# Optimization experiments

Hardware: AMD Instinct MI355X
Metric: run time of the kernel (lower is better)

## Reference

```python
import jax, jax.numpy as jnp
import numpy as np

D_WIN = 6
SIGMA = D_WIN / 2.0  # sigma = D/2
EPS = 1e-6


def _ln(x, g, b):
    m = jnp.mean(x, -1, keepdims=True)
    v = jnp.var(x, -1, keepdims=True)
    return (x - m) / jnp.sqrt(v + EPS) * g + b


def _cross_attn(q, kv, Wq, Wkv, Wproj, bproj, nh):
    # standard multi-head cross attention, no qkv bias (qkv_bias=False)
    B, S, C = q.shape
    N = kv.shape[1]
    hd = C // nh
    scale = hd ** -0.5
    qh = (q @ Wq).reshape(B, S, nh, hd).transpose(0, 2, 1, 3) * scale
    kvh = (kv @ Wkv).reshape(B, N, 2, nh, hd).transpose(2, 0, 3, 1, 4)
    k, v = kvh[0], kvh[1]
    attn = jax.nn.softmax(jnp.einsum('bhsd,bhnd->bhsn', qh, k), -1)
    x = jnp.einsum('bhsn,bhnd->bhsd', attn, v).transpose(0, 2, 1, 3).reshape(B, S, C)
    return x @ Wproj + bproj


def setup_inputs() -> dict:
    key = jax.random.key(0)
    ks = jax.random.split(key, 32)
    B, S, C, H, W = 32, 128, 384, 8, 512

    def lin(k, i, o):
        return jax.random.normal(k, (i, o), jnp.float32) * 0.02

    inp = {
        'q': jax.random.normal(ks[0], (B, S, C), jnp.float32),
        'kv': jax.random.normal(ks[1], (B, H * W, C), jnp.float32),
        # main attention linears (qkv_bias=False)
        'Wq': lin(ks[2], C, C),
        'Wkv': lin(ks[3], C, 2 * C),
        'Wproj': lin(ks[4], C, C), 'bproj': jnp.zeros((C,), jnp.float32),
        # position predictor
        'Wp_w': lin(ks[5], C, C), 'Wp_b': jnp.zeros((C,), jnp.float32),
        'vp_w': lin(ks[6], C, 1), 'vp_b': jnp.zeros((1,), jnp.float32),
        'Wqpos': lin(ks[7], C, C), 'bqpos': jnp.zeros((C,), jnp.float32),
        # simplified RCTC decoder projection
        'Wrctc': lin(ks[8], C, C), 'brctc': jnp.zeros((C,), jnp.float32),
        # pt_to_question cross attention (2 heads)
        'ca1_Wq': lin(ks[9], C, C), 'ca1_Wkv': lin(ks[10], C, 2 * C),
        'ca1_Wproj': lin(ks[11], C, C), 'ca1_bproj': jnp.zeros((C,), jnp.float32),
        # pt_to_image cross attention (2 heads)
        'ca2_Wq': lin(ks[12], C, C), 'ca2_Wkv': lin(ks[13], C, 2 * C),
        'ca2_Wproj': lin(ks[14], C, C), 'ca2_bproj': jnp.zeros((C,), jnp.float32),
        # layernorms
        'g_q1': jnp.ones((C,), jnp.float32), 'b_q1': jnp.zeros((C,), jnp.float32),
        'g_kv1': jnp.ones((C,), jnp.float32), 'b_kv1': jnp.zeros((C,), jnp.float32),
        'g_q2': jnp.ones((C,), jnp.float32), 'b_q2': jnp.zeros((C,), jnp.float32),
        'g_kv2': jnp.ones((C,), jnp.float32), 'b_kv2': jnp.zeros((C,), jnp.float32),
        'sz_h': H, 'sz_w': W,
    }
    return inp


def reference(q, kv, Wq, Wkv, Wproj, bproj, Wp_w, Wp_b, vp_w, vp_b, Wqpos, bqpos,
              Wrctc, brctc, ca1_Wq, ca1_Wkv, ca1_Wproj, ca1_bproj,
              ca2_Wq, ca2_Wkv, ca2_Wproj, ca2_bproj,
              g_q1, b_q1, g_kv1, b_kv1, g_q2, b_q2, g_kv2, b_kv2, sz_h, sz_w):
    B, N, C = kv.shape
    S = q.shape[1]
    H, W = sz_h, sz_w
    nh = 1
    hd = C // nh
    scale = hd ** -0.5

    # RCTC decoder (simplified): (B,N,C) -> (B,C,H,W) -> collapse H -> (B,W,C) -> linear
    kv_img = kv.transpose(0, 2, 1).reshape(B, C, H, W)
    dec = kv_img.mean(axis=2).transpose(0, 2, 1)  # (B, W, C)
    dec = dec @ Wrctc + brctc

    qh = (q @ Wq).reshape(B, S, nh, hd).transpose(0, 2, 1, 3) * scale  # (B,nh,S,hd)
    kvh = (dec @ Wkv).reshape(B, W, 2, nh, hd).transpose(2, 0, 3, 1, 4)
    k, v = kvh[0], kvh[1]  # (B,nh,W,hd)

    # position prediction branch
    p = q @ Wqpos + bqpos
    p = _cross_attn(_ln(p, g_q1, b_q1), _ln(q, g_kv1, b_kv1),
                    ca1_Wq, ca1_Wkv, ca1_Wproj, ca1_bproj, 2)
    p = _cross_attn(_ln(p, g_q2, b_q2), _ln(dec, g_kv2, b_kv2),
                    ca2_Wq, ca2_Wkv, ca2_Wproj, ca2_bproj, 2)
    p_t = jax.nn.sigmoid(jnp.tanh(p @ Wp_w + Wp_b) @ vp_w + vp_b) * W  # (B,S,1)

    # Gaussian window mask around predicted position
    idx = jnp.arange(W, dtype=jnp.float32)[None, None, None, :]     # (1,1,1,W)
    pexp = p_t[:, None, :, :]                                        # (B,1,S,1)
    gauss = jnp.exp(-(idx - pexp) ** 2 / (2.0 * SIGMA ** 2))         # (B,1,S,W)

    attn = jnp.einsum('bhsd,bhwd->bhsw', qh, k) * gauss
    attn = jax.nn.softmax(attn, -1)
    x = jnp.einsum('bhsw,bhwd->bhsd', attn, v).transpose(0, 2, 1, 3).reshape(B, S, C)
    return x @ Wproj + bproj
```

## Files before the change

### kernel.cpp

```cpp
#include <hip/hip_runtime.h>
#include <hip/hip_bf16.h>
#include <math.h>

#define B_ 32
#define S_ 128
#define C_ 384
#define H_ 8
#define W_ 512
#define NKV 4096

typedef __attribute__((ext_vector_type(8))) short short8;
typedef __attribute__((ext_vector_type(4))) float floatx4;

static __device__ __forceinline__ ushort f2bf(float v) {
    __hip_bfloat16 h = __float2bfloat16(v);
    return *(ushort*)&h;
}
static __device__ __forceinline__ float ldf(const float* p, size_t i) { return p[i]; }
static __device__ __forceinline__ float ldf(const ushort* p, size_t i) {
    union { uint u; float f; } c; c.u = (uint)p[i] << 16; return c.f;
}

__global__ __launch_bounds__(256) void mean_kernel(const float* __restrict__ kv,
                                                   ushort* __restrict__ dec0b) {
    int v = blockIdx.x * blockDim.x + threadIdx.x;
    int total = B_ * W_ * (C_ / 4);
    if (v >= total) return;
    int c4  = v % (C_ / 4);
    int row = v / (C_ / 4);
    int b = row / W_;
    int w = row % W_;
    const float4* src = (const float4*)kv + (size_t)(b * NKV + w) * (C_ / 4) + c4;
    float4 s = {0.f, 0.f, 0.f, 0.f};
#pragma unroll
    for (int h = 0; h < H_; ++h) {
        float4 t = src[(size_t)h * W_ * (C_ / 4)];
        s.x += t.x; s.y += t.y; s.z += t.z; s.w += t.w;
    }
    ushort4 o;
    o.x = f2bf(s.x * 0.125f); o.y = f2bf(s.y * 0.125f);
    o.z = f2bf(s.z * 0.125f); o.w = f2bf(s.w * 0.125f);
    ((ushort4*)dec0b)[v] = o;
}

__global__ __launch_bounds__(256) void cast_kernel(const float* __restrict__ in,
                                                   ushort* __restrict__ out, int n4) {
    int v = blockIdx.x * blockDim.x + threadIdx.x;
    if (v >= n4) return;
    float4 f = ((const float4*)in)[v];
    ushort4 o;
    o.x = f2bf(f.x); o.y = f2bf(f.y); o.z = f2bf(f.z); o.w = f2bf(f.w);
    ((ushort4*)out)[v] = o;
}

struct WtDesc { const float* src[12]; ushort* dst[12]; int Kd[12]; int Nd[12]; };
__global__ __launch_bounds__(256) void wtcast_kernel(WtDesc d) {
    int wi = blockIdx.y;
    int idx = blockIdx.x * 256 + threadIdx.x;
    int K = d.Kd[wi], N = d.Nd[wi];
    if (idx >= K * N) return;
    int n = idx / K, k = idx % K;
    d.dst[wi][idx] = f2bf(d.src[wi][(size_t)k * N + n]);
}

__global__ __launch_bounds__(256) void bgemm_kernel(
    const ushort* __restrict__ A, const ushort* __restrict__ Bt,
    const float* __restrict__ bias, float* __restrict__ Cout,
    ushort* __restrict__ Cbf, int M, int N, int K, float alpha, int act)
{
    __shared__ ushort As[128 * 40];
    __shared__ ushort Bs[128 * 40];
    const int tid = threadIdx.x;
    const int bm = blockIdx.y * 128, bn = blockIdx.x * 128;
    const int wav = tid >> 6, lane = tid & 63;
    const int wm = (wav >> 1) * 64, wn = (wav & 1) * 64;
    const int lrow = lane & 15, lq = lane >> 4;

    floatx4 acc[4][4] = {};

    const int sr = tid >> 1, sc0 = (tid & 1) * 16;
    const ushort* Ag = A + (size_t)(bm + sr) * K + sc0;
    const ushort* Bg = Bt + (size_t)(bn + sr) * K + sc0;
    ushort* Asw = &As[sr * 40 + sc0];
    ushort* Bsw = &Bs[sr * 40 + sc0];

    for (int k0 = 0; k0 < K; k0 += 32) {
        uint4 a0 = *(const uint4*)(Ag + k0);
        uint4 a1 = *(const uint4*)(Ag + k0 + 8);
        uint4 b0 = *(const uint4*)(Bg + k0);
        uint4 b1 = *(const uint4*)(Bg + k0 + 8);
        __syncthreads();
        *(uint4*)Asw = a0; *(uint4*)(Asw + 8) = a1;
        *(uint4*)Bsw = b0; *(uint4*)(Bsw + 8) = b1;
        __syncthreads();
        short8 af[4], bfr[4];
#pragma unroll
        for (int i = 0; i < 4; ++i)
            af[i] = *(const short8*)&As[(wm + 16 * i + lrow) * 40 + lq * 8];
#pragma unroll
        for (int j = 0; j < 4; ++j)
            bfr[j] = *(const short8*)&Bs[(wn + 16 * j + lrow) * 40 + lq * 8];
#pragma unroll
        for (int i = 0; i < 4; ++i)
#pragma unroll
            for (int j = 0; j < 4; ++j)
                acc[i][j] = __builtin_amdgcn_mfma_f32_16x16x32_bf16(af[i], bfr[j], acc[i][j], 0, 0, 0);
    }

#pragma unroll
    for (int i = 0; i < 4; ++i)
#pragma unroll
        for (int j = 0; j < 4; ++j) {
            int row = bm + wm + 16 * i + lq * 4;
            int col = bn + wn + 16 * j + lrow;
            float bv = bias ? bias[col] : 0.f;
#pragma unroll
            for (int r = 0; r < 4; ++r) {
                float v = acc[i][j][r] * alpha + bv;
                if (act == 1) v = tanhf(v);
                size_t off = (size_t)(row + r) * N + col;
                if (Cout) Cout[off] = v;
                if (Cbf) Cbf[off] = f2bf(v);
            }
        }
}

static inline void bgemm(hipStream_t st, const ushort* A, const ushort* Bt,
                         const float* bias, float* Cout, ushort* Cbf,
                         int M, int N, int K, float alpha, int act) {
    dim3 grid(N / 128, M / 128), block(256);
    bgemm_kernel<<<grid, block, 0, st>>>(A, Bt, bias, Cout, Cbf, M, N, K, alpha, act);
}

struct BGArgs {
    const ushort* A; const ushort* Bt;
    const float* bias; float* outF; ushort* outB;
    int lda, ldb, ldo;
    long AsB, BsB, OsB;
    int AsH, BsH, OsH;
    int K, NH;
    float alpha; int act;
};
__global__ __launch_bounds__(256) void battn_kernel(BGArgs g) {
    __shared__ ushort As[64 * 40];
    __shared__ ushort Bs[64 * 40];
    const int bn = blockIdx.x * 64, bm = blockIdx.y * 64;
    const int bat = blockIdx.z, bb = bat / g.NH, hh = bat % g.NH;
    const ushort* A  = g.A  + (size_t)bb * g.AsB + (size_t)hh * g.AsH;
    const ushort* Bt = g.Bt + (size_t)bb * g.BsB + (size_t)hh * g.BsH;
    const int tid = threadIdx.x;
    const int wav = tid >> 6, lane = tid & 63;
    const int lrow = lane & 15, lq = lane >> 4;
    const int sr = tid >> 2, sc0 = (tid & 3) * 8;
    const ushort* Ag = A  + (size_t)(bm + sr) * g.lda + sc0;
    const ushort* Bg = Bt + (size_t)(bn + sr) * g.ldb + sc0;
    ushort* Asw = &As[sr * 40 + sc0];
    ushort* Bsw = &Bs[sr * 40 + sc0];

    floatx4 acc[4] = {};

    for (int k0 = 0; k0 < g.K; k0 += 32) {
        uint4 a = *(const uint4*)(Ag + k0);
        uint4 b = *(const uint4*)(Bg + k0);
        __syncthreads();
        *(uint4*)Asw = a; *(uint4*)Bsw = b;
        __syncthreads();
        short8 af = *(const short8*)&As[(wav * 16 + lrow) * 40 + lq * 8];
#pragma unroll
        for (int j = 0; j < 4; ++j) {
            short8 bf = *(const short8*)&Bs[(16 * j + lrow) * 40 + lq * 8];
            acc[j] = __builtin_amdgcn_mfma_f32_16x16x32_bf16(af, bf, acc[j], 0, 0, 0);
        }
    }

#pragma unroll
    for (int j = 0; j < 4; ++j) {
        int col = bn + 16 * j + lrow;
        float bv = g.bias ? g.bias[col] : 0.f;
        int row0 = bm + wav * 16 + lq * 4;
#pragma unroll
        for (int r = 0; r < 4; ++r) {
            float v = acc[j][r] * g.alpha + bv;
            if (g.act == 1) v = tanhf(v);
            size_t off = (size_t)bb * g.OsB + (size_t)hh * g.OsH
                       + (size_t)(row0 + r) * g.ldo + col;
            if (g.outF) g.outF[off] = v;
            if (g.outB) g.outB[off] = f2bf(v);
        }
    }
}

static inline void battn(hipStream_t st, const ushort* A, const ushort* Bt,
                         const float* bias, float* outF, ushort* outB,
                         int M, int N, int K, float alpha, int act,
                         int lda, long AsB, int AsH,
                         int ldb, long BsB, int BsH,
                         int ldo, long OsB, int OsH,
                         int NH, int nbat) {
    BGArgs g;
    g.A = A; g.Bt = Bt; g.bias = bias; g.outF = outF; g.outB = outB;
    g.lda = lda; g.ldb = ldb; g.ldo = ldo;
    g.AsB = AsB; g.BsB = BsB; g.OsB = OsB;
    g.AsH = AsH; g.BsH = BsH; g.OsH = OsH;
    g.K = K; g.NH = NH; g.alpha = alpha; g.act = act;
    dim3 grid(N / 64, M / 64, nbat);
    battn_kernel<<<grid, 256, 0, st>>>(g);
}

static inline void bgemm64(hipStream_t st, const ushort* A, const ushort* Bt,
                           const float* bias, float* outF, ushort* outB,
                           int M, int N, int K, float alpha, int act) {
    battn(st, A, Bt, bias, outF, outB, M, N, K, alpha, act,
          K, 0, 0, K, 0, 0, N, 0, 0, 1, 1);
}

template <typename T>
__global__ __launch_bounds__(128) void ln_kernel(const T* __restrict__ X,
    const float* __restrict__ g, const float* __restrict__ bb,
    ushort* __restrict__ Y) {
    int row = blockIdx.x;
    const T* x = X + (size_t)row * C_;
    ushort* y = Y + (size_t)row * C_;
    int t = threadIdx.x;
    float v0 = ldf(x, t), v1 = ldf(x, t + 128), v2 = ldf(x, t + 256);
    float s = v0 + v1 + v2, sq = v0 * v0 + v1 * v1 + v2 * v2;
    __shared__ float rs[128], rq[128];
    rs[t] = s; rq[t] = sq; __syncthreads();
    if (t < 64) {
        s = rs[t] + rs[t + 64]; sq = rq[t] + rq[t + 64];
        for (int o = 32; o; o >>= 1) { s += __shfl_down(s, o); sq += __shfl_down(sq, o); }
        if (t == 0) { rs[0] = s; rq[0] = sq; }
    }
    __syncthreads();
    float mean = rs[0] * (1.0f / C_);
    float var  = rq[0] * (1.0f / C_) - mean * mean;
    float inv  = rsqrtf(var + 1e-6f);
    y[t]       = f2bf((v0 - mean) * inv * g[t]       + bb[t]);
    y[t + 128] = f2bf((v1 - mean) * inv * g[t + 128] + bb[t + 128]);
    y[t + 256] = f2bf((v2 - mean) * inv * g[t + 256] + bb[t + 256]);
}

template <int NW, int GAUSS>
__global__ __launch_bounds__(256) void softmax_kernel(
    const float* __restrict__ sc, const float* __restrict__ ptv,
    ushort* __restrict__ P)
{
    int row = blockIdx.x * 4 + (threadIdx.x >> 6);
    int lane = threadIdx.x & 63;
    const float* s = sc + (size_t)row * NW;
    float pcen = GAUSS ? ptv[row] : 0.f;
    float vals[NW / 64];
    float m = -1e30f;
#pragma unroll
    for (int i = 0; i < NW / 64; ++i) {
        int w = lane + 64 * i;
        float v = s[w];
        if (GAUSS) { float dw = (float)w - pcen; v *= expf(dw * dw * (-1.0f / 18.0f)); }
        vals[i] = v; m = fmaxf(m, v);
    }
#pragma unroll
    for (int o = 32; o; o >>= 1) m = fmaxf(m, __shfl_xor(m, o));
    float sum = 0.f;
#pragma unroll
    for (int i = 0; i < NW / 64; ++i) { vals[i] = expf(vals[i] - m); sum += vals[i]; }
#pragma unroll
    for (int o = 32; o; o >>= 1) sum += __shfl_xor(sum, o);
    float rinv = 1.0f / sum;
    ushort* op = P + (size_t)row * NW;
#pragma unroll
    for (int i = 0; i < NW / 64; ++i) op[lane + 64 * i] = f2bf(vals[i] * rinv);
}

__global__ __launch_bounds__(256) void vtrans_kernel(
    const ushort* __restrict__ kvb, ushort* __restrict__ vt,
    int Nw, int C2, int CC)
{
    int b = blockIdx.z;
    int w0 = blockIdx.x * 32, c0 = blockIdx.y * 32;
    __shared__ ushort t[32][33];
    int tid = threadIdx.x;
    int wl = tid >> 3, c4 = (tid & 7) * 4;
    ushort4 v = *(const ushort4*)&kvb[((size_t)b * Nw + w0 + wl) * C2 + CC + c0 + c4];
    t[wl][c4] = v.x; t[wl][c4 + 1] = v.y; t[wl][c4 + 2] = v.z; t[wl][c4 + 3] = v.w;
    __syncthreads();
    int dl = tid >> 3, w4 = (tid & 7) * 4;
    ushort4 o;
    o.x = t[w4][dl]; o.y = t[w4 + 1][dl]; o.z = t[w4 + 2][dl]; o.w = t[w4 + 3][dl];
    *(ushort4*)&vt[((size_t)b * CC + c0 + dl) * Nw + w0 + w4] = o;
}

__global__ __launch_bounds__(128) void pt_kernel(const float* __restrict__ T,
    const float* __restrict__ vpw, const float* __restrict__ vpb,
    float* __restrict__ out) {
    int row = blockIdx.x;
    int t = threadIdx.x;
    const float* x = T + (size_t)row * C_;
    float s = x[t] * vpw[t] + x[t + 128] * vpw[t + 128] + x[t + 256] * vpw[t + 256];
    __shared__ float red[128];
    red[t] = s; __syncthreads();
    if (t < 64) {
        s = red[t] + red[t + 64];
        for (int o = 32; o; o >>= 1) s += __shfl_down(s, o);
        if (t == 0) {
            float z = s + vpb[0];
            out[row] = 512.0f / (1.0f + expf(-z));
        }
    }
}

extern "C" void kernel_launch(void* const* d_in, const int* in_sizes, int n_in,
                              void* d_out, int out_size, void* d_ws, size_t ws_size,
                              hipStream_t stream) {
    const float* q     = (const float*)d_in[0];
    const float* kv    = (const float*)d_in[1];
    const float* Wq    = (const float*)d_in[2];
    const float* Wkv   = (const float*)d_in[3];
    const float* Wproj = (const float*)d_in[4];
    const float* bproj = (const float*)d_in[5];
    const float* Wp_w  = (const float*)d_in[6];
    const float* Wp_b  = (const float*)d_in[7];
    const float* vp_w  = (const float*)d_in[8];
    const float* vp_b  = (const float*)d_in[9];
    const float* Wqpos = (const float*)d_in[10];
    const float* bqpos = (const float*)d_in[11];
    const float* Wrctc = (const float*)d_in[12];
    const float* brctc = (const float*)d_in[13];
    const float* ca1_Wq    = (const float*)d_in[14];
    const float* ca1_Wkv   = (const float*)d_in[15];
    const float* ca1_Wproj = (const float*)d_in[16];
    const float* ca1_bproj = (const float*)d_in[17];
    const float* ca2_Wq    = (const float*)d_in[18];
    const float* ca2_Wkv   = (const float*)d_in[19];
    const float* ca2_Wproj = (const float*)d_in[20];
    const float* ca2_bproj = (const float*)d_in[21];
    const float* g_q1  = (const float*)d_in[22];
    const float* b_q1  = (const float*)d_in[23];
    const float* g_kv1 = (const float*)d_in[24];
    const float* b_kv1 = (const float*)d_in[25];
    const float* g_q2  = (const float*)d_in[26];
    const float* b_q2  = (const float*)d_in[27];
    const float* g_kv2 = (const float*)d_in[28];
    const float* b_kv2 = (const float*)d_in[29];
    float* out = (float*)d_out;
    float* ws  = (float*)d_ws;

    ushort* dec0b = (ushort*)(ws);
    ushort* wb    = (ushort*)(ws + 3145728);
    ushort* qb    = (ushort*)(ws + 4251648);
    ushort* decb  = (ushort*)(ws + 5038080);
    ushort* qhb   = (ushort*)(ws + 8183808);
    float*  p     = ws + 8970240;
    ushort* pb    = (ushort*)(ws + 10543104);
    float*  t1    = ws + 11329536;
    ushort* t1b   = (ushort*)(ws + 12902400);
    ushort* t2b   = (ushort*)(ws + 13688832);
    ushort* qpb   = (ushort*)(ws + 16834560);
    ushort* kvb   = (ushort*)(ws + 17620992);
    ushort* vt    = (ushort*)(ws + 23912448);
    float*  sc    = ws + 27058176;
    ushort* Pb    = (ushort*)(ws + 31252480);
    ushort* xb    = (ushort*)(ws + 33349632);
    float*  ptb   = ws + 34136064;

    ushort* wbWq     = wb;
    ushort* wbWqpos  = wb + 147456;
    ushort* wbWrctc  = wb + 294912;
    ushort* wbC1Wq   = wb + 442368;
    ushort* wbC1Wp   = wb + 589824;
    ushort* wbC2Wq   = wb + 737280;
    ushort* wbC2Wp   = wb + 884736;
    ushort* wbWpw    = wb + 1032192;
    ushort* wbWproj  = wb + 1179648;
    ushort* wbWkv    = wb + 1327104;
    ushort* wbC1Wkv  = wb + 1622016;
    ushort* wbC2Wkv  = wb + 1916928;

    const float rs384 = 0.05103103630798288f;
    const float rs192 = 0.07216878364870323f;

    mean_kernel<<<(B_ * W_ * (C_ / 4) + 255) / 256, 256, 0, stream>>>(kv, dec0b);
    {
        WtDesc d;
        const float* s_[12] = {Wq, Wqpos, Wrctc, ca1_Wq, ca1_Wproj, ca2_Wq, ca2_Wproj,
                               Wp_w, Wproj, Wkv, ca1_Wkv, ca2_Wkv};
        ushort* t_[12] = {wbWq, wbWqpos, wbWrctc, wbC1Wq, wbC1Wp, wbC2Wq, wbC2Wp,
                          wbWpw, wbWproj, wbWkv, wbC1Wkv, wbC2Wkv};
        for (int i = 0; i < 12; ++i) {
            d.src[i] = s_[i]; d.dst[i] = t_[i];
            d.Kd[i] = 384; d.Nd[i] = (i >= 9) ? 768 : 384;
        }
        dim3 grid((294912 + 255) / 256, 12);
        wtcast_kernel<<<grid, 256, 0, stream>>>(d);
        cast_kernel<<<(393216 + 255) / 256, 256, 0, stream>>>(q, qb, 393216);
    }
    bgemm(stream, dec0b, wbWrctc, brctc, nullptr, decb, B_ * W_, 384, 384, 1.f, 0);
    bgemm64(stream, qb, wbWq, nullptr, nullptr, qhb, B_ * S_, 384, 384, rs384, 0);
    bgemm64(stream, qb, wbWqpos, bqpos, p, nullptr, B_ * S_, 384, 384, 1.f, 0);
    ln_kernel<float><<<B_ * S_, 128, 0, stream>>>(p, g_q1, b_q1, t1b);
    ln_kernel<float><<<B_ * S_, 128, 0, stream>>>(q, g_kv1, b_kv1, t2b);
    bgemm64(stream, t1b, wbC1Wq, nullptr, nullptr, qpb, B_ * S_, 384, 384, rs192, 0);
    bgemm64(stream, t2b, wbC1Wkv, nullptr, nullptr, kvb, B_ * S_, 768, 384, 1.f, 0);
    {
        dim3 gt(S_ / 32, C_ / 32, B_);
        vtrans_kernel<<<gt, 256, 0, stream>>>(kvb, vt, S_, 768, 384);
    }
    battn(stream, qpb, kvb, nullptr, sc, nullptr, 128, 128, 192, 1.f, 0,
          384, (long)S_ * 384, 192,
          768, (long)S_ * 768, 192,
          128, (long)2 * S_ * 128, S_ * 128, 2, 64);
    softmax_kernel<128, 0><<<(B_ * 2 * S_) / 4, 256, 0, stream>>>(sc, nullptr, Pb);
    battn(stream, Pb, vt, nullptr, nullptr, xb, 128, 192, 128, 1.f, 0,
          128, (long)2 * S_ * 128, S_ * 128,
          128, (long)C_ * S_, 192 * S_,
          384, (long)S_ * 384, 192, 2, 64);
    bgemm64(stream, xb, wbC1Wp, ca1_bproj, p, nullptr, B_ * S_, 384, 384, 1.f, 0);
    ln_kernel<float><<<B_ * S_, 128, 0, stream>>>(p, g_q2, b_q2, t1b);
    ln_kernel<ushort><<<B_ * W_, 128, 0, stream>>>(decb, g_kv2, b_kv2, t2b);
    bgemm64(stream, t1b, wbC2Wq, nullptr, nullptr, qpb, B_ * S_, 384, 384, rs192, 0);
    bgemm(stream, t2b, wbC2Wkv, nullptr, nullptr, kvb, B_ * W_, 768, 384, 1.f, 0);
    {
        dim3 gt(W_ / 32, C_ / 32, B_);
        vtrans_kernel<<<gt, 256, 0, stream>>>(kvb, vt, W_, 768, 384);
    }
    battn(stream, qpb, kvb, nullptr, sc, nullptr, 128, 512, 192, 1.f, 0,
          384, (long)S_ * 384, 192,
          768, (long)W_ * 768, 192,
          512, (long)2 * S_ * 512, S_ * 512, 2, 64);
    softmax_kernel<512, 0><<<(B_ * 2 * S_) / 4, 256, 0, stream>>>(sc, nullptr, Pb);
    battn(stream, Pb, vt, nullptr, nullptr, xb, 128, 192, 512, 1.f, 0,
          512, (long)2 * S_ * 512, S_ * 512,
          512, (long)C_ * W_, 192 * W_,
          384, (long)S_ * 384, 192, 2, 64);
    bgemm64(stream, xb, wbC2Wp, ca2_bproj, p, pb, B_ * S_, 384, 384, 1.f, 0);
    bgemm64(stream, pb, wbWpw, Wp_b, t1, nullptr, B_ * S_, 384, 384, 1.f, 1);
    pt_kernel<<<B_ * S_, 128, 0, stream>>>(t1, vp_w, vp_b, ptb);
    bgemm(stream, decb, wbWkv, nullptr, nullptr, kvb, B_ * W_, 768, 384, 1.f, 0);
    {
        dim3 gt(W_ / 32, C_ / 32, B_);
        vtrans_kernel<<<gt, 256, 0, stream>>>(kvb, vt, W_, 768, 384);
    }
    battn(stream, qhb, kvb, nullptr, sc, nullptr, 128, 512, 384, 1.f, 0,
          384, (long)S_ * 384, 0,
          768, (long)W_ * 768, 0,
          512, (long)S_ * 512, 0, 1, 32);
    softmax_kernel<512, 1><<<(B_ * S_) / 4, 256, 0, stream>>>(sc, ptb, Pb);
    battn(stream, Pb, vt, nullptr, nullptr, xb, 128, 384, 512, 1.f, 0,
          512, (long)S_ * 512, 0,
          512, (long)C_ * W_, 0,
          384, (long)S_ * 384, 0, 1, 32);
    bgemm64(stream, xb, wbWproj, bproj, out, nullptr, B_ * S_, 384, 384, 1.f, 0);
}
```

Baseline: 614.0 us.

## Fuse softmax, V-transpose, LayerNorm pairs and weight casts into neighbouring kernels

Removes the standalone softmax and V-transpose kernels. The softmax row max and sum and the exp/normalize now run inside the P·V GEMM A-load, and the Gaussian mask is applied in the score GEMM epilogue. The KV projection epilogue writes K and transposed V directly, the two LayerNorm launches per stage and the q-cast/weight-cast launches are merged, and the Wq/Wqpos GEMMs are concatenated into one N=768 launch. This cuts launch count and intermediate round trips. In exchange, every P·V tile recomputes exp over its rows, each block redundantly recomputes row statistics, and the transposed-V stores from the GEMM epilogue are scattered.

```diff
diff --git a/kernel.cpp b/kernel.cpp
--- a/kernel.cpp
+++ b/kernel.cpp
@@ -43,30 +43,25 @@
     ((ushort4*)dec0b)[v] = o;
 }
 
-__global__ __launch_bounds__(256) void cast_kernel(const float* __restrict__ in,
-                                                   ushort* __restrict__ out, int n4) {
-    int v = blockIdx.x * blockDim.x + threadIdx.x;
-    if (v >= n4) return;
-    float4 f = ((const float4*)in)[v];
-    ushort4 o;
-    o.x = f2bf(f.x); o.y = f2bf(f.y); o.z = f2bf(f.z); o.w = f2bf(f.w);
-    ((ushort4*)out)[v] = o;
-}
-
-struct WtDesc { const float* src[12]; ushort* dst[12]; int Kd[12]; int Nd[12]; };
-__global__ __launch_bounds__(256) void wtcast_kernel(WtDesc d) {
-    int wi = blockIdx.y;
-    int idx = blockIdx.x * 256 + threadIdx.x;
-    int K = d.Kd[wi], N = d.Nd[wi];
-    if (idx >= K * N) return;
-    int n = idx / K, k = idx % K;
-    d.dst[wi][idx] = f2bf(d.src[wi][(size_t)k * N + n]);
+struct WtD2 { const float* src[13]; ushort* dst[13]; int off[14]; };
+__global__ __launch_bounds__(256) void wtcast_kernel(WtD2 d) {
+    int gid = blockIdx.x * 256 + threadIdx.x;
+    if (gid >= d.off[13]) return;
+    int j = 0;
+    while (j < 12 && gid >= d.off[j + 1]) ++j;
+    int idx = gid - d.off[j];
+    if (j == 12) { d.dst[12][idx] = f2bf(d.src[12][idx]); return; }
+    const int K = 384;
+    int N = (j >= 9) ? 768 : 384;
+    int n = idx / K, k = idx - n * K;
+    d.dst[j][idx] = f2bf(d.src[j][(size_t)k * N + n]);
 }
 
 __global__ __launch_bounds__(256) void bgemm_kernel(
     const ushort* __restrict__ A, const ushort* __restrict__ Bt,
     const float* __restrict__ bias, float* __restrict__ Cout,
-    ushort* __restrict__ Cbf, int M, int N, int K, float alpha, int act)
+    ushort* __restrict__ Cbf, ushort* __restrict__ kdst, ushort* __restrict__ vtdst,
+    int nw, int nws, int M, int N, int K, float alpha, int act)
 {
     __shared__ ushort As[128 * 40];
     __shared__ ushort Bs[128 * 40];
@@ -111,59 +106,99 @@
     for (int i = 0; i < 4; ++i)
 #pragma unroll
         for (int j = 0; j < 4; ++j) {
-            int row = bm + wm + 16 * i + lq * 4;
+            int row0 = bm + wm + 16 * i + lq * 4;
             int col = bn + wn + 16 * j + lrow;
             float bv = bias ? bias[col] : 0.f;
 #pragma unroll
             for (int r = 0; r < 4; ++r) {
                 float v = acc[i][j][r] * alpha + bv;
                 if (act == 1) v = tanhf(v);
-                size_t off = (size_t)(row + r) * N + col;
-                if (Cout) Cout[off] = v;
-                if (Cbf) Cbf[off] = f2bf(v);
+                int row = row0 + r;
+                if (kdst) {
+                    int b = row >> nws, w = row & (nw - 1);
+                    if (col < 384) kdst[(size_t)row * 384 + col] = f2bf(v);
+                    else vtdst[((size_t)b * 384 + (col - 384)) * (size_t)nw + w] = f2bf(v);
+                } else {
+                    size_t off = (size_t)row * N + col;
+                    if (Cout) Cout[off] = v;
+                    if (Cbf) Cbf[off] = f2bf(v);
+                }
             }
         }
 }
 
-static inline void bgemm(hipStream_t st, const ushort* A, const ushort* Bt,
-                         const float* bias, float* Cout, ushort* Cbf,
-                         int M, int N, int K, float alpha, int act) {
-    dim3 grid(N / 128, M / 128), block(256);
-    bgemm_kernel<<<grid, block, 0, st>>>(A, Bt, bias, Cout, Cbf, M, N, K, alpha, act);
-}
-
 struct BGArgs {
-    const ushort* A; const ushort* Bt;
-    const float* bias; float* outF; ushort* outB;
+    const ushort* A; const float* Af; const ushort* Bt;
+    const float* bias; float* outF; ushort* outB; ushort* outS;
     int lda, ldb, ldo;
     long AsB, BsB, OsB;
     int AsH, BsH, OsH;
     int K, NH;
-    float alpha; int act;
+    float alpha; int act; int mode; int gauss;
+    const float* ptv;
 };
 __global__ __launch_bounds__(256) void battn_kernel(BGArgs g) {
     __shared__ ushort As[64 * 40];
     __shared__ ushort Bs[64 * 40];
+    __shared__ float rowm[64], rowr[64];
     const int bn = blockIdx.x * 64, bm = blockIdx.y * 64;
     const int bat = blockIdx.z, bb = bat / g.NH, hh = bat % g.NH;
-    const ushort* A  = g.A  + (size_t)bb * g.AsB + (size_t)hh * g.AsH;
-    const ushort* Bt = g.Bt + (size_t)bb * g.BsB + (size_t)hh * g.BsH;
     const int tid = threadIdx.x;
     const int wav = tid >> 6, lane = tid & 63;
     const int lrow = lane & 15, lq = lane >> 4;
     const int sr = tid >> 2, sc0 = (tid & 3) * 8;
-    const ushort* Ag = A  + (size_t)(bm + sr) * g.lda + sc0;
-    const ushort* Bg = Bt + (size_t)(bn + sr) * g.ldb + sc0;
+
+    const ushort* Bg = g.Bt + (size_t)bb * g.BsB + (size_t)hh * g.BsH
+                     + (size_t)(bn + sr) * g.ldb + sc0;
     ushort* Asw = &As[sr * 40 + sc0];
     ushort* Bsw = &Bs[sr * 40 + sc0];
 
+    const ushort* Ag = nullptr;
+    const float* Agf = nullptr;
+    if (g.mode == 2) {
+        const float* base = g.Af + (size_t)bb * g.AsB + (size_t)hh * g.AsH;
+        Agf = base + (size_t)(bm + sr) * g.lda + sc0;
+        for (int r = wav; r < 64; r += 4) {
+            const float* srow = base + (size_t)(bm + r) * g.lda;
+            float mx = -1e30f;
+            for (int c = lane; c < g.K; c += 64) mx = fmaxf(mx, srow[c]);
+#pragma unroll
+            for (int o = 32; o; o >>= 1) mx = fmaxf(mx, __shfl_xor(mx, o));
+            float sm = 0.f;
+            for (int c = lane; c < g.K; c += 64) sm += expf(srow[c] - mx);
+#pragma unroll
+            for (int o = 32; o; o >>= 1) sm += __shfl_xor(sm, o);
+            if (lane == 0) { rowm[r] = mx; rowr[r] = 1.0f / sm; }
+        }
+        __syncthreads();
+    } else {
+        Ag = g.A + (size_t)bb * g.AsB + (size_t)hh * g.AsH
+           + (size_t)(bm + sr) * g.lda + sc0;
+    }
+
     floatx4 acc[4] = {};
 
     for (int k0 = 0; k0 < g.K; k0 += 32) {
-        uint4 a = *(const uint4*)(Ag + k0);
         uint4 b = *(const uint4*)(Bg + k0);
+        union { ushort us[8]; uint4 v; } ap;
+        if (g.mode == 2) {
+            float4 f0 = *(const float4*)(Agf + k0);
+            float4 f1 = *(const float4*)(Agf + k0 + 4);
+            float m = rowm[sr], rv = rowr[sr];
+            ap.us[0] = f2bf(expf(f0.x - m) * rv);
+            ap.us[1] = f2bf(expf(f0.y - m) * rv);
+            ap.us[2] = f2bf(expf(f0.z - m) * rv);
+            ap.us[3] = f2bf(expf(f0.w - m) * rv);
+            ap.us[4] = f2bf(expf(f1.x - m) * rv);
+            ap.us[5] = f2bf(expf(f1.y - m) * rv);
+            ap.us[6] = f2bf(expf(f1.z - m) * rv);
+            ap.us[7] = f2bf(expf(f1.w - m) * rv);
+        } else {
+            ap.v = *(const uint4*)(Ag + k0);
+        }
         __syncthreads();
-        *(uint4*)Asw = a; *(uint4*)Bsw = b;
+        *(uint4*)Asw = ap.v;
+        *(uint4*)Bsw = b;
         __syncthreads();
         short8 af = *(const short8*)&As[(wav * 16 + lrow) * 40 + lq * 8];
 #pragma unroll
@@ -176,33 +211,47 @@
 #pragma unroll
     for (int j = 0; j < 4; ++j) {
         int col = bn + 16 * j + lrow;
-        float bv = g.bias ? g.bias[col] : 0.f;
         int row0 = bm + wav * 16 + lq * 4;
 #pragma unroll
         for (int r = 0; r < 4; ++r) {
-            float v = acc[j][r] * g.alpha + bv;
+            float v = acc[j][r] * g.alpha;
+            int row = row0 + r;
+            if (g.mode == 1) {
+                if (col < 384) g.outS[(size_t)row * 384 + col] = f2bf(v);
+                else g.outF[(size_t)row * 384 + (col - 384)] = v + g.bias[col - 384];
+                continue;
+            }
+            if (g.bias) v += g.bias[col];
             if (g.act == 1) v = tanhf(v);
+            if (g.gauss) {
+                float dw = (float)col - g.ptv[bb * S_ + row];
+                v *= expf(dw * dw * (-1.0f / 18.0f));
+            }
             size_t off = (size_t)bb * g.OsB + (size_t)hh * g.OsH
-                       + (size_t)(row0 + r) * g.ldo + col;
+                       + (size_t)row * g.ldo + col;
             if (g.outF) g.outF[off] = v;
             if (g.outB) g.outB[off] = f2bf(v);
         }
     }
 }
 
-static inline void battn(hipStream_t st, const ushort* A, const ushort* Bt,
-                         const float* bias, float* outF, ushort* outB,
-                         int M, int N, int K, float alpha, int act,
+static inline void battn(hipStream_t st, const ushort* A, const float* Af,
+                         const ushort* Bt, const float* bias,
+                         float* outF, ushort* outB, ushort* outS,
+                         int M, int N, int K, float alpha, int act, int mode, int gauss,
+                         const float* ptv,
                          int lda, long AsB, int AsH,
                          int ldb, long BsB, int BsH,
                          int ldo, long OsB, int OsH,
                          int NH, int nbat) {
     BGArgs g;
-    g.A = A; g.Bt = Bt; g.bias = bias; g.outF = outF; g.outB = outB;
+    g.A = A; g.Af = Af; g.Bt = Bt; g.bias = bias;
+    g.outF = outF; g.outB = outB; g.outS = outS;
     g.lda = lda; g.ldb = ldb; g.ldo = ldo;
     g.AsB = AsB; g.BsB = BsB; g.OsB = OsB;
     g.AsH = AsH; g.BsH = BsH; g.OsH = OsH;
-    g.K = K; g.NH = NH; g.alpha = alpha; g.act = act;
+    g.K = K; g.NH = NH; g.alpha = alpha; g.act = act; g.mode = mode;
+    g.gauss = gauss; g.ptv = ptv;
     dim3 grid(N / 64, M / 64, nbat);
     battn_kernel<<<grid, 256, 0, st>>>(g);
 }
@@ -210,19 +259,34 @@
 static inline void bgemm64(hipStream_t st, const ushort* A, const ushort* Bt,
                            const float* bias, float* outF, ushort* outB,
                            int M, int N, int K, float alpha, int act) {
-    battn(st, A, Bt, bias, outF, outB, M, N, K, alpha, act,
-          K, 0, 0, K, 0, 0, N, 0, 0, 1, 1);
-}
-
-template <typename T>
-__global__ __launch_bounds__(128) void ln_kernel(const T* __restrict__ X,
-    const float* __restrict__ g, const float* __restrict__ bb,
-    ushort* __restrict__ Y) {
-    int row = blockIdx.x;
-    const T* x = X + (size_t)row * C_;
-    ushort* y = Y + (size_t)row * C_;
+    battn(st, A, nullptr, Bt, bias, outF, outB, nullptr, M, N, K, alpha, act, 0, 0,
+          nullptr, K, 0, 0, K, 0, 0, N, 0, 0, 1, 1);
+}
+
+struct LN2Args {
+    const float* X1; const float* g1; const float* b1; ushort* Y1; int n1;
+    const void* X2; int x2bf; const float* g2; const float* b2; ushort* Y2;
+};
+__global__ __launch_bounds__(128) void ln2_kernel(LN2Args a) {
+    int blk = blockIdx.x;
     int t = threadIdx.x;
-    float v0 = ldf(x, t), v1 = ldf(x, t + 128), v2 = ldf(x, t + 256);
+    float v0, v1, v2;
+    const float *g, *bb; ushort* y;
+    if (blk < a.n1) {
+        const float* x = a.X1 + (size_t)blk * C_;
+        v0 = x[t]; v1 = x[t + 128]; v2 = x[t + 256];
+        g = a.g1; bb = a.b1; y = a.Y1 + (size_t)blk * C_;
+    } else {
+        int row = blk - a.n1;
+        if (a.x2bf) {
+            const ushort* x = (const ushort*)a.X2 + (size_t)row * C_;
+            v0 = ldf(x, t); v1 = ldf(x, t + 128); v2 = ldf(x, t + 256);
+        } else {
+            const float* x = (const float*)a.X2 + (size_t)row * C_;
+            v0 = x[t]; v1 = x[t + 128]; v2 = x[t + 256];
+        }
+        g = a.g2; bb = a.b2; y = a.Y2 + (size_t)row * C_;
+    }
     float s = v0 + v1 + v2, sq = v0 * v0 + v1 * v1 + v2 * v2;
     __shared__ float rs[128], rq[128];
     rs[t] = s; rq[t] = sq; __syncthreads();
@@ -238,55 +302,6 @@
     y[t]       = f2bf((v0 - mean) * inv * g[t]       + bb[t]);
     y[t + 128] = f2bf((v1 - mean) * inv * g[t + 128] + bb[t + 128]);
     y[t + 256] = f2bf((v2 - mean) * inv * g[t + 256] + bb[t + 256]);
-}
-
-template <int NW, int GAUSS>
-__global__ __launch_bounds__(256) void softmax_kernel(
-    const float* __restrict__ sc, const float* __restrict__ ptv,
-    ushort* __restrict__ P)
-{
-    int row = blockIdx.x * 4 + (threadIdx.x >> 6);
-    int lane = threadIdx.x & 63;
-    const float* s = sc + (size_t)row * NW;
-    float pcen = GAUSS ? ptv[row] : 0.f;
-    float vals[NW / 64];
-    float m = -1e30f;
-#pragma unroll
-    for (int i = 0; i < NW / 64; ++i) {
-        int w = lane + 64 * i;
-        float v = s[w];
-        if (GAUSS) { float dw = (float)w - pcen; v *= expf(dw * dw * (-1.0f / 18.0f)); }
-        vals[i] = v; m = fmaxf(m, v);
-    }
-#pragma unroll
-    for (int o = 32; o; o >>= 1) m = fmaxf(m, __shfl_xor(m, o));
-    float sum = 0.f;
-#pragma unroll
-    for (int i = 0; i < NW / 64; ++i) { vals[i] = expf(vals[i] - m); sum += vals[i]; }
-#pragma unroll
-    for (int o = 32; o; o >>= 1) sum += __shfl_xor(sum, o);
-    float rinv = 1.0f / sum;
-    ushort* op = P + (size_t)row * NW;
-#pragma unroll
-    for (int i = 0; i < NW / 64; ++i) op[lane + 64 * i] = f2bf(vals[i] * rinv);
-}
-
-__global__ __launch_bounds__(256) void vtrans_kernel(
-    const ushort* __restrict__ kvb, ushort* __restrict__ vt,
-    int Nw, int C2, int CC)
-{
-    int b = blockIdx.z;
-    int w0 = blockIdx.x * 32, c0 = blockIdx.y * 32;
-    __shared__ ushort t[32][33];
-    int tid = threadIdx.x;
-    int wl = tid >> 3, c4 = (tid & 7) * 4;
-    ushort4 v = *(const ushort4*)&kvb[((size_t)b * Nw + w0 + wl) * C2 + CC + c0 + c4];
-    t[wl][c4] = v.x; t[wl][c4 + 1] = v.y; t[wl][c4 + 2] = v.z; t[wl][c4 + 3] = v.w;
-    __syncthreads();
-    int dl = tid >> 3, w4 = (tid & 7) * 4;
-    ushort4 o;
-    o.x = t[w4][dl]; o.y = t[w4 + 1][dl]; o.z = t[w4 + 2][dl]; o.w = t[w4 + 3][dl];
-    *(ushort4*)&vt[((size_t)b * CC + c0 + dl) * Nw + w0 + w4] = o;
 }
 
 __global__ __launch_bounds__(128) void pt_kernel(const float* __restrict__ T,
@@ -355,15 +370,13 @@
     ushort* t1b   = (ushort*)(ws + 12902400);
     ushort* t2b   = (ushort*)(ws + 13688832);
     ushort* qpb   = (ushort*)(ws + 16834560);
-    ushort* kvb   = (ushort*)(ws + 17620992);
-    ushort* vt    = (ushort*)(ws + 23912448);
-    float*  sc    = ws + 27058176;
-    ushort* Pb    = (ushort*)(ws + 31252480);
-    ushort* xb    = (ushort*)(ws + 33349632);
-    float*  ptb   = ws + 34136064;
-
-    ushort* wbWq     = wb;
-    ushort* wbWqpos  = wb + 147456;
+    ushort* kb    = (ushort*)(ws + 17620992);
+    ushort* vt    = (ushort*)(ws + 20766720);
+    float*  sc    = ws + 23912448;
+    ushort* xb    = (ushort*)(ws + 28106752);
+    float*  ptb   = ws + 28893184;
+
+    ushort* wbQQ     = wb;
     ushort* wbWrctc  = wb + 294912;
     ushort* wbC1Wq   = wb + 442368;
     ushort* wbC1Wp   = wb + 589824;
@@ -379,74 +392,98 @@
     const float rs192 = 0.07216878364870323f;
 
     mean_kernel<<<(B_ * W_ * (C_ / 4) + 255) / 256, 256, 0, stream>>>(kv, dec0b);
-    {
-        WtDesc d;
-        const float* s_[12] = {Wq, Wqpos, Wrctc, ca1_Wq, ca1_Wproj, ca2_Wq, ca2_Wproj,
-                               Wp_w, Wproj, Wkv, ca1_Wkv, ca2_Wkv};
-        ushort* t_[12] = {wbWq, wbWqpos, wbWrctc, wbC1Wq, wbC1Wp, wbC2Wq, wbC2Wp,
-                          wbWpw, wbWproj, wbWkv, wbC1Wkv, wbC2Wkv};
-        for (int i = 0; i < 12; ++i) {
-            d.src[i] = s_[i]; d.dst[i] = t_[i];
-            d.Kd[i] = 384; d.Nd[i] = (i >= 9) ? 768 : 384;
-        }
-        dim3 grid((294912 + 255) / 256, 12);
-        wtcast_kernel<<<grid, 256, 0, stream>>>(d);
-        cast_kernel<<<(393216 + 255) / 256, 256, 0, stream>>>(q, qb, 393216);
-    }
-    bgemm(stream, dec0b, wbWrctc, brctc, nullptr, decb, B_ * W_, 384, 384, 1.f, 0);
-    bgemm64(stream, qb, wbWq, nullptr, nullptr, qhb, B_ * S_, 384, 384, rs384, 0);
-    bgemm64(stream, qb, wbWqpos, bqpos, p, nullptr, B_ * S_, 384, 384, 1.f, 0);
-    ln_kernel<float><<<B_ * S_, 128, 0, stream>>>(p, g_q1, b_q1, t1b);
-    ln_kernel<float><<<B_ * S_, 128, 0, stream>>>(q, g_kv1, b_kv1, t2b);
-    bgemm64(stream, t1b, wbC1Wq, nullptr, nullptr, qpb, B_ * S_, 384, 384, rs192, 0);
-    bgemm64(stream, t2b, wbC1Wkv, nullptr, nullptr, kvb, B_ * S_, 768, 384, 1.f, 0);
-    {
-        dim3 gt(S_ / 32, C_ / 32, B_);
-        vtrans_kernel<<<gt, 256, 0, stream>>>(kvb, vt, S_, 768, 384);
-    }
-    battn(stream, qpb, kvb, nullptr, sc, nullptr, 128, 128, 192, 1.f, 0,
+
+    {
+        WtD2 d;
+        const float* s_[13] = {Wq, Wqpos, Wrctc, ca1_Wq, ca1_Wproj, ca2_Wq, ca2_Wproj,
+                               Wp_w, Wproj, Wkv, ca1_Wkv, ca2_Wkv, q};
+        ushort* t_[13] = {wbQQ, wbQQ + 147456, wbWrctc, wbC1Wq, wbC1Wp, wbC2Wq, wbC2Wp,
+                          wbWpw, wbWproj, wbWkv, wbC1Wkv, wbC2Wkv, qb};
+        int cnt[13] = {147456,147456,147456,147456,147456,147456,147456,147456,147456,
+                       294912,294912,294912, 1572864};
+        int acc = 0;
+        for (int i = 0; i < 13; ++i) { d.src[i] = s_[i]; d.dst[i] = t_[i]; d.off[i] = acc; acc += cnt[i]; }
+        d.off[13] = acc;
+        wtcast_kernel<<<(acc + 255) / 256, 256, 0, stream>>>(d);
+    }
+
+    battn(stream, qb, nullptr, wbQQ, bqpos, p, nullptr, qhb,
+          B_ * S_, 768, 384, 1.f, 0, 1, 0, nullptr,
+          384, 0, 0, 384, 0, 0, 384, 0, 0, 1, 1);
+
+    {
+        dim3 grid(384 / 128, (B_ * W_) / 128);
+        bgemm_kernel<<<grid, 256, 0, stream>>>(dec0b, wbWrctc, brctc, nullptr, decb,
+                                               nullptr, nullptr, 0, 0,
+                                               B_ * W_, 384, 384, 1.f, 0);
+    }
+
+    {
+        LN2Args a = {p, g_q1, b_q1, t1b, B_ * S_, q, 0, g_kv1, b_kv1, t2b};
+        ln2_kernel<<<2 * B_ * S_, 128, 0, stream>>>(a);
+    }
+    bgemm64(stream, t1b, wbC1Wq, nullptr, nullptr, qpb, B_ * S_, 384, 384, 1.f, 0);
+    {
+        dim3 grid(768 / 128, (B_ * S_) / 128);
+        bgemm_kernel<<<grid, 256, 0, stream>>>(t2b, wbC1Wkv, nullptr, nullptr, nullptr,
+                                               kb, vt, 128, 7,
+                                               B_ * S_, 768, 384, 1.f, 0);
+    }
+    battn(stream, qpb, nullptr, kb, nullptr, sc, nullptr, nullptr,
+          S_, 128, 192, rs192, 0, 0, 0, nullptr,
           384, (long)S_ * 384, 192,
-          768, (long)S_ * 768, 192,
+          384, (long)S_ * 384, 192,
           128, (long)2 * S_ * 128, S_ * 128, 2, 64);
-    softmax_kernel<128, 0><<<(B_ * 2 * S_) / 4, 256, 0, stream>>>(sc, nullptr, Pb);
-    battn(stream, Pb, vt, nullptr, nullptr, xb, 128, 192, 128, 1.f, 0,
+    battn(stream, nullptr, sc, vt, nullptr, nullptr, xb, nullptr,
+          S_, 192, 128, 1.f, 0, 2, 0, nullptr,
           128, (long)2 * S_ * 128, S_ * 128,
           128, (long)C_ * S_, 192 * S_,
           384, (long)S_ * 384, 192, 2, 64);
     bgemm64(stream, xb, wbC1Wp, ca1_bproj, p, nullptr, B_ * S_, 384, 384, 1.f, 0);
-    ln_kernel<float><<<B_ * S_, 128, 0, stream>>>(p, g_q2, b_q2, t1b);
-    ln_kernel<ushort><<<B_ * W_, 128, 0, stream>>>(decb, g_kv2, b_kv2, t2b);
-    bgemm64(stream, t1b, wbC2Wq, nullptr, nullptr, qpb, B_ * S_, 384, 384, rs192, 0);
-    bgemm(stream, t2b, wbC2Wkv, nullptr, nullptr, kvb, B_ * W_, 768, 384, 1.f, 0);
-    {
-        dim3 gt(W_ / 32, C_ / 32, B_);
-        vtrans_kernel<<<gt, 256, 0, stream>>>(kvb, vt, W_, 768, 384);
-    }
-    battn(stream, qpb, kvb, nullptr, sc, nullptr, 128, 512, 192, 1.f, 0,
+
+    {
+        LN2Args a = {p, g_q2, b_q2, t1b, B_ * S_, decb, 1, g_kv2, b_kv2, t2b};
+        ln2_kernel<<<B_ * S_ + B_ * W_, 128, 0, stream>>>(a);
+    }
+    bgemm64(stream, t1b, wbC2Wq, nullptr, nullptr, qpb, B_ * S_, 384, 384, 1.f, 0);
+    {
+        dim3 grid(768 / 128, (B_ * W_) / 128);
+        bgemm_kernel<<<grid, 256, 0, stream>>>(t2b, wbC2Wkv, nullptr, nullptr, nullptr,
+                                               kb, vt, 512, 9,
+                                               B_ * W_, 768, 384, 1.f, 0);
+    }
+    battn(stream, qpb, nullptr, kb, nullptr, sc, nullptr, nullptr,
+          S_, 512, 192, rs192, 0, 0, 0, nullptr,
           384, (long)S_ * 384, 192,
-          768, (long)W_ * 768, 192,
+          384, (long)W_ * 384, 192,
           512, (long)2 * S_ * 512, S_ * 512, 2, 64);
-    softmax_kernel<512, 0><<<(B_ * 2 * S_) / 4, 256, 0, stream>>>(sc, nullptr, Pb);
-    battn(stream, Pb, vt, nullptr, nullptr, xb, 128, 192, 512, 1.f, 0,
+    battn(stream, nullptr, sc, vt, nullptr, nullptr, xb, nullptr,
+          S_, 192, 512, 1.f, 0, 2, 0, nullptr,
           512, (long)2 * S_ * 512, S_ * 512,
           512, (long)C_ * W_, 192 * W_,
           384, (long)S_ * 384, 192, 2, 64);
     bgemm64(stream, xb, wbC2Wp, ca2_bproj, p, pb, B_ * S_, 384, 384, 1.f, 0);
+
     bgemm64(stream, pb, wbWpw, Wp_b, t1, nullptr, B_ * S_, 384, 384, 1.f, 1);
     pt_kernel<<<B_ * S_, 128, 0, stream>>>(t1, vp_w, vp_b, ptb);
-    bgemm(stream, decb, wbWkv, nullptr, nullptr, kvb, B_ * W_, 768, 384, 1.f, 0);
-    {
-        dim3 gt(W_ / 32, C_ / 32, B_);
-        vtrans_kernel<<<gt, 256, 0, stream>>>(kvb, vt, W_, 768, 384);
-    }
-    battn(stream, qhb, kvb, nullptr, sc, nullptr, 128, 512, 384, 1.f, 0,
+
+    {
+        dim3 grid(768 / 128, (B_ * W_) / 128);
+        bgemm_kernel<<<grid, 256, 0, stream>>>(decb, wbWkv, nullptr, nullptr, nullptr,
+                                               kb, vt, 512, 9,
+                                               B_ * W_, 768, 384, 1.f, 0);
+    }
+
+    battn(stream, qhb, nullptr, kb, nullptr, sc, nullptr, nullptr,
+          S_, 512, 384, rs384, 0, 0, 1, ptb,
           384, (long)S_ * 384, 0,
-          768, (long)W_ * 768, 0,
+          384, (long)W_ * 384, 0,
           512, (long)S_ * 512, 0, 1, 32);
-    softmax_kernel<512, 1><<<(B_ * S_) / 4, 256, 0, stream>>>(sc, ptb, Pb);
-    battn(stream, Pb, vt, nullptr, nullptr, xb, 128, 384, 512, 1.f, 0,
+    battn(stream, nullptr, sc, vt, nullptr, nullptr, xb, nullptr,
+          S_, 384, 512, 1.f, 0, 2, 0, nullptr,
           512, (long)S_ * 512, 0,
           512, (long)C_ * W_, 0,
           384, (long)S_ * 384, 0, 1, 32);
+
     bgemm64(stream, xb, wbWproj, bproj, out, nullptr, B_ * S_, 384, 384, 1.f, 0);
 }
```

New measurement: 777.0 us. 26.6% more time.
